# Kernel optimization log

Measured on AMD Instinct MI355X. Metric: run time of the kernel, lower is better.

Reference implementation:

```python
import jax, jax.numpy as jnp
import numpy as np

OBS_DIM, ACT_DIM, HID_DIM, FEAT = 256, 32, 1024, 512
T_STEPS, BATCH = 64, 512
LOG2PI = float(np.log(2.0 * np.pi))


def _mlp(h, w0, b0, w1, b1, w2, b2):
    # 2 hidden elu layers + linear head (MLPDecoder mean; fix_std Normal, std=1)
    x = jax.nn.elu(h @ w0.T + b0)
    x = jax.nn.elu(x @ w1.T + b1)
    return x @ w2.T + b2


def _gru(x, h, w_ih, w_hh, b_ih, b_hh):
    # torch.nn.GRUCell semantics
    gi = x @ w_ih.T + b_ih
    gh = h @ w_hh.T + b_hh
    i_r, i_z, i_n = jnp.split(gi, 3, axis=-1)
    h_r, h_z, h_n = jnp.split(gh, 3, axis=-1)
    r = jax.nn.sigmoid(i_r + h_r)
    z = jax.nn.sigmoid(i_z + h_z)
    n = jnp.tanh(i_n + r * h_n)
    return (1.0 - z) * n + z * h


def setup_inputs() -> dict:
    key = jax.random.key(0)
    ks = jax.random.split(key, 20)
    d = {}
    d['obs'] = jax.random.normal(ks[0], (T_STEPS, BATCH, OBS_DIM), jnp.float32)
    d['action'] = jax.random.normal(ks[1], (T_STEPS, BATCH, ACT_DIM), jnp.float32)
    d['reward'] = jax.random.normal(ks[2], (T_STEPS, BATCH, 1), jnp.float32)
    in_dim = OBS_DIM + ACT_DIM
    s = lambda fan_in: 1.0 / np.sqrt(fan_in)
    d['gru_w_ih'] = jax.random.normal(ks[3], (3 * HID_DIM, in_dim), jnp.float32) * s(in_dim)
    d['gru_w_hh'] = jax.random.normal(ks[4], (3 * HID_DIM, HID_DIM), jnp.float32) * s(HID_DIM)
    d['gru_b_ih'] = jnp.zeros((3 * HID_DIM,), jnp.float32)
    d['gru_b_hh'] = jnp.zeros((3 * HID_DIM,), jnp.float32)
    for name, out_dim, base in (('obs', OBS_DIM, 5), ('rew', 1, 11)):
        d[f'{name}_w0'] = jax.random.normal(ks[base], (FEAT, HID_DIM), jnp.float32) * s(HID_DIM)
        d[f'{name}_b0'] = jnp.zeros((FEAT,), jnp.float32)
        d[f'{name}_w1'] = jax.random.normal(ks[base + 1], (FEAT, FEAT), jnp.float32) * s(FEAT)
        d[f'{name}_b1'] = jnp.zeros((FEAT,), jnp.float32)
        d[f'{name}_w2'] = jax.random.normal(ks[base + 2], (out_dim, FEAT), jnp.float32) * s(FEAT)
        d[f'{name}_b2'] = jnp.zeros((out_dim,), jnp.float32)
    return d


def reference(obs, action, reward,
              gru_w_ih, gru_w_hh, gru_b_ih, gru_b_hh,
              obs_w0, obs_b0, obs_w1, obs_b1, obs_w2, obs_b2,
              rew_w0, rew_b0, rew_w1, rew_b1, rew_w2, rew_b2):
    T, B = obs.shape[0], obs.shape[1]

    def normal_logprob_sum(x, mean):
        # Normal(mean, std=1): -0.5*(x-mean)^2 - 0.5*log(2*pi), summed
        return -0.5 * jnp.sum((x - mean) ** 2 + LOG2PI)

    h0 = _gru(jnp.concatenate([obs[0], jnp.zeros_like(action[0])], axis=1),
              jnp.zeros((B, HID_DIM), obs.dtype),
              gru_w_ih, gru_w_hh, gru_b_ih, gru_b_hh)

    def step(h, xs):
        obs_t, act_t, rew_t = xs
        obs_mean = _mlp(h, obs_w0, obs_b0, obs_w1, obs_b1, obs_w2, obs_b2)
        lp_obs = normal_logprob_sum(obs_t, obs_mean)
        rew_mean = _mlp(h, rew_w0, rew_b0, rew_w1, rew_b1, rew_w2, rew_b2)
        lp_rew = normal_logprob_sum(rew_t, rew_mean)
        # feed predicted obs (mode) + ground-truth action back into the GRU
        x = jnp.concatenate([obs_mean, act_t], axis=1)
        h_next = _gru(x, h, gru_w_ih, gru_w_hh, gru_b_ih, gru_b_hh)
        return h_next, (obs_mean, rew_mean, lp_obs, lp_rew)

    _, (pre_obs, pre_reward, lp_obs, lp_rew) = jax.lax.scan(
        step, h0, (obs, action, reward))

    denom = jnp.asarray(T * B, obs.dtype)
    pre_obs_loss = -jnp.sum(lp_obs) / denom
    pre_reward_loss = -jnp.sum(lp_rew) / denom
    loss = pre_obs_loss + pre_reward_loss  # action_mimic=False -> action loss is 0
    return loss, pre_obs, pre_reward
```

## Files before the change

### kernel.cpp

```cpp
#include <hip/hip_runtime.h>
#include <stdint.h>

#define T_STEPS 64
#define BATCH   512
#define OBS_DIM 256
#define ACT_DIM 32
#define HID     1024
#define FEAT    512
#define GDIM    3072
#define KIH     288
#define NBLK    256
#define GMEMB   32
#define LOG2PI  1.8378770664093453f
#define HWREG_XCC_ID 14356

typedef __attribute__((ext_vector_type(8))) short  short8;
typedef __attribute__((ext_vector_type(4))) float  floatx4;
typedef __attribute__((ext_vector_type(4))) unsigned int uintx4;
typedef unsigned long long ull;

__device__ __forceinline__ float bf2f(unsigned int u) {
    return __uint_as_float(u << 16);
}
__device__ __forceinline__ unsigned int f2bf(float f) {
    unsigned int u = __float_as_uint(f);
    return (u + 0x7FFFu + ((u >> 16) & 1u)) >> 16;
}
__device__ __forceinline__ float elu1(float x)  { return x > 0.f ? x : expm1f(x); }
__device__ __forceinline__ float sigm(float x)  { return 1.f / (1.f + expf(-x)); }

__device__ __forceinline__ unsigned int dev_ld(const unsigned int* p) {
    return __hip_atomic_load(p, __ATOMIC_RELAXED, __HIP_MEMORY_SCOPE_AGENT);
}
__device__ __forceinline__ ull dev_ld64(const ull* p) {
    return __hip_atomic_load(p, __ATOMIC_RELAXED, __HIP_MEMORY_SCOPE_AGENT);
}
__device__ __forceinline__ void dev_st(unsigned int* p, unsigned int v) {
    __hip_atomic_store(p, v, __ATOMIC_RELAXED, __HIP_MEMORY_SCOPE_AGENT);
}
__device__ __forceinline__ float dev_ldf(const float* p) {
    return __uint_as_float(dev_ld((const unsigned int*)p));
}

template<bool COH>
__device__ __forceinline__ unsigned int a_ld(const unsigned int* p) {
    return COH ? dev_ld(p) : *p;
}
template<bool COH>
__device__ __forceinline__ ull a_ld64(const ull* p) {
    return COH ? dev_ld64(p) : *p;
}
template<bool COH>
__device__ __forceinline__ void a_st(unsigned int* p, unsigned int v) {
    if (COH) dev_st(p, v); else *p = v;
}

struct ParamsReal {
    const float* obs; const float* action; const float* reward;
    const float* b_ih; const float* b_hh;
    const float* b1o; const float* b1r; const float* b2o; const float* b2r;
    const unsigned short* Ws1; const unsigned short* Wih;
    const unsigned short* W1o; const unsigned short* W1r;
    const unsigned short* W2o; const unsigned short* w2r;
    const float* bias_s1;
    unsigned short* Z1[2]; unsigned short* Z2[2]; unsigned short* Xbuf[2];
    unsigned short* hbf[2]; unsigned short* GHb[2]; float* h[2];
    float* accum; float* out;
    int* bar;
};
#define P ParamsReal

__device__ __forceinline__ void bar_fast() {
    asm volatile("" ::: "memory");
    __builtin_amdgcn_s_barrier();
    asm volatile("" ::: "memory");
}
__device__ __forceinline__ void bar_lds() {
    asm volatile("s_waitcnt lgkmcnt(0)" ::: "memory");
    __builtin_amdgcn_s_barrier();
    asm volatile("" ::: "memory");
}

__device__ __forceinline__ void gbar(int* cnt, int* gen, int& epoch, int members) {
    __syncthreads();
    if (threadIdx.x == 0) {
        __builtin_amdgcn_fence(__ATOMIC_RELEASE, "workgroup");
        epoch++;
        int prev = __hip_atomic_fetch_add(cnt, 1, __ATOMIC_RELAXED,
                                          __HIP_MEMORY_SCOPE_AGENT);
        if (prev == members * epoch - 1) {
            __hip_atomic_store(gen, epoch, __ATOMIC_RELAXED,
                               __HIP_MEMORY_SCOPE_AGENT);
        } else {
            while (__hip_atomic_load(gen, __ATOMIC_RELAXED,
                                     __HIP_MEMORY_SCOPE_AGENT) < epoch)
                __builtin_amdgcn_s_sleep(2);
        }
        __builtin_amdgcn_fence(__ATOMIC_ACQUIRE, "workgroup");
    }
    __syncthreads();
}

template<bool COH>
__device__ __forceinline__ void s1_stage(const P& p, unsigned short* lds,
                                         int g, int m,
                                         const unsigned short* hbf_r,
                                         unsigned short* Z1_w,
                                         unsigned short* GHb_w) {
    const int tid = threadIdx.x, lane = tid & 63, wv = tid >> 6;
    const int wr = wv & 1, wc = wv >> 1, fr = lane & 15, fq = lane >> 4;
    const int rowg = g * 64, col0 = m * 128;
    unsigned short* ldsA = lds;
    unsigned short* ldsB = lds + 64 * 136;

    floatx4 acc[2][4];
    floatx4 z4 = {0.f, 0.f, 0.f, 0.f};
#pragma unroll
    for (int mi = 0; mi < 2; ++mi)
#pragma unroll
        for (int n = 0; n < 4; ++n) acc[mi][n] = z4;

    const ull* Aq = (const ull*)(hbf_r + (size_t)rowg * HID);
    const unsigned short* Bg = p.Ws1 + (size_t)col0 * HID;

    ull apf[8];
#pragma unroll
    for (int j = 0; j < 8; ++j) { int f = tid + 256 * j;
        apf[j] = a_ld64<COH>(Aq + (size_t)(f >> 5) * 256 + (f & 31)); }
    uintx4 rb0[4], rb1[4];
#pragma unroll
    for (int i = 0; i < 4; ++i) { int c = tid + 256 * i;
        const unsigned short* bp = Bg + (size_t)(c >> 3) * HID + ((c & 7) << 3);
        rb0[i] = __builtin_nontemporal_load((const uintx4*)bp);
        rb1[i] = __builtin_nontemporal_load((const uintx4*)(bp + 64)); }

#define S1_MFMA(ASUB)                                                          \
    {                                                                          \
        _Pragma("unroll")                                                      \
        for (int ks = 0; ks < 2; ++ks) {                                       \
            short8 af[2], bf8[4];                                              \
            _Pragma("unroll")                                                  \
            for (int mi = 0; mi < 2; ++mi)                                     \
                af[mi] = *(const short8*)(ldsA + (wr * 32 + mi * 16 + fr) * 136 + (ASUB) + ks * 32 + fq * 8); \
            _Pragma("unroll")                                                  \
            for (int n = 0; n < 4; ++n)                                        \
                bf8[n] = *(const short8*)(ldsB + (wc * 64 + n * 16 + fr) * 72 + ks * 32 + fq * 8); \
            _Pragma("unroll")                                                  \
            for (int mi = 0; mi < 2; ++mi)                                     \
                _Pragma("unroll")                                              \
                for (int n = 0; n < 4; ++n)                                    \
                    acc[mi][n] = __builtin_amdgcn_mfma_f32_16x16x32_bf16(      \
                        af[mi], bf8[n], acc[mi][n], 0, 0, 0);                  \
        }                                                                      \
    }

    for (int it2 = 0; it2 < 8; ++it2) {
        bar_fast();
#pragma unroll
        for (int j = 0; j < 8; ++j) { int f = tid + 256 * j;
            *(ull*)(ldsA + (size_t)(f >> 5) * 136 + ((f & 31) << 2)) = apf[j]; }
#pragma unroll
        for (int i = 0; i < 4; ++i) { int c = tid + 256 * i;
            *(uintx4*)(ldsB + (c >> 3) * 72 + ((c & 7) << 3)) = rb0[i]; }
        bar_lds();
        if (it2 < 7) {
            int c2 = it2 + 1;
#pragma unroll
            for (int j = 0; j < 8; ++j) { int f = tid + 256 * j;
                apf[j] = a_ld64<COH>(Aq + (size_t)(f >> 5) * 256 + c2 * 32 + (f & 31)); }
            int k0n = (2 * it2 + 2) * 64;
#pragma unroll
            for (int i = 0; i < 4; ++i) { int c = tid + 256 * i;
                rb0[i] = __builtin_nontemporal_load((const uintx4*)
                    (Bg + (size_t)(c >> 3) * HID + k0n + ((c & 7) << 3))); }
        }
        S1_MFMA(0);
        bar_fast();
#pragma unroll
        for (int i = 0; i < 4; ++i) { int c = tid + 256 * i;
            *(uintx4*)(ldsB + (c >> 3) * 72 + ((c & 7) << 3)) = rb1[i]; }
        bar_lds();
        if (it2 < 7) {
            int k0n = (2 * it2 + 3) * 64;
#pragma unroll
            for (int i = 0; i < 4; ++i) { int c = tid + 256 * i;
                rb1[i] = __builtin_nontemporal_load((const uintx4*)
                    (Bg + (size_t)(c >> 3) * HID + k0n + ((c & 7) << 3))); }
        }
        S1_MFMA(64);
    }
#undef S1_MFMA

    const bool isZ1 = (col0 < 1024);
#pragma unroll
    for (int mi = 0; mi < 2; ++mi)
#pragma unroll
        for (int n = 0; n < 4; ++n)
#pragma unroll
            for (int j = 0; j < 4; ++j) {
                int row = rowg + wr * 32 + mi * 16 + fq * 4 + j;
                int col = col0 + wc * 64 + n * 16 + fr;
                float v = acc[mi][n][j] + p.bias_s1[col];
                unsigned int ow = f2bf(isZ1 ? elu1(v) : v);
                unsigned int pr = __shfl_xor(ow, 1, 64);
                if (!(fr & 1)) {
                    unsigned int pk = ow | (pr << 16);
                    if (isZ1)
                        a_st<COH>((unsigned int*)(Z1_w + row * HID + col), pk);
                    else
                        a_st<COH>((unsigned int*)GHb_w + (size_t)row * 1536 + ((col - 1024) >> 1), pk);
                }
            }
}

template<bool COH>
__device__ __forceinline__ void s2_stage(const P& p, unsigned short* lds,
                                         int g, int m,
                                         const unsigned short* Z1_r,
                                         unsigned short* Z2_w) {
    const int tid = threadIdx.x, lane = tid & 63, wv = tid >> 6;
    const int wr = wv & 1, wc = wv >> 1, fr = lane & 15, fq = lane >> 4;
    const int rowg = g * 64;
    const int z = m >> 4, col0 = (m & 15) * 32;
    unsigned short* ldsA = lds;
    unsigned short* ldsB = lds + 64 * 136;

    floatx4 acc[2];
    floatx4 z4 = {0.f, 0.f, 0.f, 0.f};
    acc[0] = z4; acc[1] = z4;

    const ull* Aq = (const ull*)(Z1_r + (size_t)rowg * HID + z * FEAT);
    const unsigned short* Bg = (z ? p.W1r : p.W1o) + (size_t)col0 * FEAT;
    const float* bias = z ? p.b1r : p.b1o;

    ull apf[8];
#pragma unroll
    for (int j = 0; j < 8; ++j) { int f = tid + 256 * j;
        apf[j] = a_ld64<COH>(Aq + (size_t)(f >> 5) * 256 + (f & 31)); }
    const unsigned short* bp0 = Bg + (size_t)(tid >> 3) * FEAT + ((tid & 7) << 3);
    uintx4 rb0 = *(const uintx4*)(bp0);
    uintx4 rb1 = *(const uintx4*)(bp0 + 64);

#define S2_MFMA(ASUB)                                                          \
    {                                                                          \
        _Pragma("unroll")                                                      \
        for (int ks = 0; ks < 2; ++ks) {                                       \
            short8 bf8 = *(const short8*)(ldsB + (wc * 16 + fr) * 72 + ks * 32 + fq * 8); \
            _Pragma("unroll")                                                  \
            for (int mi = 0; mi < 2; ++mi) {                                   \
                short8 af = *(const short8*)(ldsA + (wr * 32 + mi * 16 + fr) * 136 + (ASUB) + ks * 32 + fq * 8); \
                acc[mi] = __builtin_amdgcn_mfma_f32_16x16x32_bf16(af, bf8, acc[mi], 0, 0, 0); \
            }                                                                  \
        }                                                                      \
    }

    for (int it2 = 0; it2 < 4; ++it2) {
        bar_fast();
#pragma unroll
        for (int j = 0; j < 8; ++j) { int f = tid + 256 * j;
            *(ull*)(ldsA + (size_t)(f >> 5) * 136 + ((f & 31) << 2)) = apf[j]; }
        *(uintx4*)(ldsB + (tid >> 3) * 72 + ((tid & 7) << 3)) = rb0;
        bar_lds();
        if (it2 < 3) {
            int c2 = it2 + 1;
#pragma unroll
            for (int j = 0; j < 8; ++j) { int f = tid + 256 * j;
                apf[j] = a_ld64<COH>(Aq + (size_t)(f >> 5) * 256 + c2 * 32 + (f & 31)); }
            rb0 = *(const uintx4*)(bp0 + (2 * it2 + 2) * 64);
        }
        S2_MFMA(0);
        bar_fast();
        *(uintx4*)(ldsB + (tid >> 3) * 72 + ((tid & 7) << 3)) = rb1;
        bar_lds();
        if (it2 < 3) rb1 = *(const uintx4*)(bp0 + (2 * it2 + 3) * 64);
        S2_MFMA(64);
    }
#undef S2_MFMA

#pragma unroll
    for (int mi = 0; mi < 2; ++mi)
#pragma unroll
        for (int j = 0; j < 4; ++j) {
            int row = rowg + wr * 32 + mi * 16 + fq * 4 + j;
            int col = col0 + wc * 16 + fr;
            float v = acc[mi][j] + bias[col];
            unsigned int ow = f2bf(elu1(v));
            unsigned int pr = __shfl_xor(ow, 1, 64);
            if (!(fr & 1))
                a_st<COH>((unsigned int*)(Z2_w + row * HID + z * FEAT + col), ow | (pr << 16));
        }
}

template<bool COH>
__device__ __forceinline__ void s3_stage(const P& p, unsigned short* lds,
                                         int g, int m, int t,
                                         const unsigned short* Z2_r,
                                         unsigned short* Xbuf_w) {
    const int tid = threadIdx.x, lane = tid & 63, wv = tid >> 6;
    const int wr = wv & 1, wc = wv >> 1, fr = lane & 15, fq = lane >> 4;
    const int rowg = g * 64;

    if (m < 8) {
        const int col0 = m * 32;
        unsigned short* ldsA = lds;
        unsigned short* ldsB = lds + 64 * 136;
        floatx4 acc[2];
        floatx4 z4 = {0.f, 0.f, 0.f, 0.f};
        acc[0] = z4; acc[1] = z4;

        const ull* Aq = (const ull*)(Z2_r + (size_t)rowg * HID);
        const unsigned short* Bg = p.W2o + (size_t)col0 * FEAT;

        ull apf[8];
#pragma unroll
        for (int j = 0; j < 8; ++j) { int f = tid + 256 * j;
            apf[j] = a_ld64<COH>(Aq + (size_t)(f >> 5) * 256 + (f & 31)); }
        const unsigned short* bp0 = Bg + (size_t)(tid >> 3) * FEAT + ((tid & 7) << 3);
        uintx4 rb0 = *(const uintx4*)(bp0);
        uintx4 rb1 = *(const uintx4*)(bp0 + 64);

#define S3_MFMA(ASUB)                                                          \
        {                                                                      \
            _Pragma("unroll")                                                  \
            for (int ks = 0; ks < 2; ++ks) {                                   \
                short8 bf8 = *(const short8*)(ldsB + (wc * 16 + fr) * 72 + ks * 32 + fq * 8); \
                _Pragma("unroll")                                              \
                for (int mi = 0; mi < 2; ++mi) {                               \
                    short8 af = *(const short8*)(ldsA + (wr * 32 + mi * 16 + fr) * 136 + (ASUB) + ks * 32 + fq * 8); \
                    acc[mi] = __builtin_amdgcn_mfma_f32_16x16x32_bf16(af, bf8, acc[mi], 0, 0, 0); \
                }                                                              \
            }                                                                  \
        }

        for (int it2 = 0; it2 < 4; ++it2) {
            bar_fast();
#pragma unroll
            for (int j = 0; j < 8; ++j) { int f = tid + 256 * j;
                *(ull*)(ldsA + (size_t)(f >> 5) * 136 + ((f & 31) << 2)) = apf[j]; }
            *(uintx4*)(ldsB + (tid >> 3) * 72 + ((tid & 7) << 3)) = rb0;
            bar_lds();
            if (it2 < 3) {
                int c2 = it2 + 1;
#pragma unroll
                for (int j = 0; j < 8; ++j) { int f = tid + 256 * j;
                    apf[j] = a_ld64<COH>(Aq + (size_t)(f >> 5) * 256 + c2 * 32 + (f & 31)); }
                rb0 = *(const uintx4*)(bp0 + (2 * it2 + 2) * 64);
            }
            S3_MFMA(0);
            bar_fast();
            *(uintx4*)(ldsB + (tid >> 3) * 72 + ((tid & 7) << 3)) = rb1;
            bar_lds();
            if (it2 < 3) rb1 = *(const uintx4*)(bp0 + (2 * it2 + 3) * 64);
            S3_MFMA(64);
        }
#undef S3_MFMA

        const int col = col0 + wc * 16 + fr;
        const float b2oc = p.b2o[col];
        float lsum = 0.f;
#pragma unroll
        for (int mi = 0; mi < 2; ++mi)
#pragma unroll
            for (int j = 0; j < 4; ++j) {
                int row = rowg + wr * 32 + mi * 16 + fq * 4 + j;
                float mval = acc[mi][j] + b2oc;
                size_t oidx = (size_t)t * BATCH * OBS_DIM + (size_t)row * OBS_DIM + col;
                __builtin_nontemporal_store(mval, p.out + 1 + oidx);
                unsigned int ow = f2bf(mval);
                unsigned int pr = __shfl_xor(ow, 1, 64);
                if (!(fr & 1))
                    a_st<COH>((unsigned int*)(Xbuf_w + row * KIH + col), ow | (pr << 16));
                float d = __builtin_nontemporal_load(p.obs + oidx) - mval;
                lsum += d * d;
            }
#pragma unroll
        for (int off = 32; off > 0; off >>= 1) lsum += __shfl_down(lsum, off, 64);
        if (lane == 0) atomicAdd(p.accum + 0, lsum);
    } else if (m == 8) {
        for (int e = tid; e < 64 * 16; e += 256) {
            int row = rowg + (e >> 4), cp = (e & 15) * 2;
            const float* ap = p.action + ((size_t)t * BATCH + row) * ACT_DIM + cp;
            unsigned int lo = f2bf(__builtin_nontemporal_load(ap));
            unsigned int hi = f2bf(__builtin_nontemporal_load(ap + 1));
            a_st<COH>((unsigned int*)(Xbuf_w + row * KIH + OBS_DIM + cp), lo | (hi << 16));
        }
    } else if (m >= 16) {
        const int row = rowg + (m - 16) * 4 + wv;
        const ull* zq = (const ull*)(Z2_r + (size_t)row * HID + FEAT) + lane * 2;
        ull z0 = a_ld64<COH>(zq);
        ull z1 = a_ld64<COH>(zq + 1);
        short8 w8 = *(const short8*)(p.w2r + lane * 8);
        float s = 0.f;
#pragma unroll
        for (int k = 0; k < 4; ++k) {
            unsigned int u = (unsigned int)(z0 >> (16 * k)) & 0xFFFFu;
            s += bf2f(u) * bf2f((unsigned int)(unsigned short)w8[k]);
        }
#pragma unroll
        for (int k = 0; k < 4; ++k) {
            unsigned int u = (unsigned int)(z1 >> (16 * k)) & 0xFFFFu;
            s += bf2f(u) * bf2f((unsigned int)(unsigned short)w8[4 + k]);
        }
#pragma unroll
        for (int off = 32; off > 0; off >>= 1) s += __shfl_down(s, off, 64);
        if (lane == 0) {
            float mm = s + p.b2r[0];
            __builtin_nontemporal_store(
                mm, p.out + 1 + (size_t)T_STEPS * BATCH * OBS_DIM + (size_t)t * BATCH + row);
            float d = __builtin_nontemporal_load(p.reward + (size_t)t * BATCH + row) - mm;
            atomicAdd(p.accum + 1, d * d);
        }
    }
}

template<bool COH>
__device__ __forceinline__ void s4_stage(const P& p, unsigned short* lds,
                                         int g, int m, int use_gh,
                                         const unsigned short* Xbuf_r,
                                         const unsigned short* GHb_r,
                                         const float* h_r,
                                         float* h_w, unsigned short* hbf_w) {
    const int tid = threadIdx.x, lane = tid & 63, wv = tid >> 6;
    const int wr = wv & 1, wc = wv >> 1, fr = lane & 15, fq = lane >> 4;
    const int rowg = g * 64;
    const int col0 = m * 32;
    unsigned short* ldsA = lds;
    unsigned short* ldsB = lds + 64 * 104;

    floatx4 acc[3][2];
    floatx4 z4 = {0.f, 0.f, 0.f, 0.f};
#pragma unroll
    for (int g3 = 0; g3 < 3; ++g3) { acc[g3][0] = z4; acc[g3][1] = z4; }

    const ull* Xq = (const ull*)(Xbuf_r + (size_t)rowg * KIH);
    ull apf[6];
#pragma unroll
    for (int j = 0; j < 6; ++j) { int f = tid + 256 * j;
        apf[j] = a_ld64<COH>(Xq + (size_t)(f / 24) * 72 + (f % 24)); }

    uintx4 wpfA[5], wpfB[5];
#pragma unroll
    for (int j = 0; j < 5; ++j) { int f = tid + 256 * j;
        if (f < 1152) { int r = f / 12, ko = (f - r * 12) * 8;
            const unsigned short* wp =
                p.Wih + (size_t)((r >> 5) * HID + col0 + (r & 31)) * KIH + ko;
            wpfA[j] = __builtin_nontemporal_load((const uintx4*)wp);
            wpfB[j] = __builtin_nontemporal_load((const uintx4*)(wp + 96)); } }

#pragma unroll
    for (int c = 0; c < 3; ++c) {
        bar_fast();
#pragma unroll
        for (int j = 0; j < 6; ++j) { int f = tid + 256 * j;
            *(ull*)(ldsA + (size_t)(f / 24) * 104 + ((f % 24) << 2)) = apf[j]; }
#pragma unroll
        for (int j = 0; j < 5; ++j) { int f = tid + 256 * j;
            if (f < 1152) { int r = f / 12, ko = (f - r * 12) * 8;
                *(uintx4*)(ldsB + r * 104 + ko) = (c & 1) ? wpfB[j] : wpfA[j]; } }
        bar_lds();
        if (c < 2) {
#pragma unroll
            for (int j = 0; j < 6; ++j) { int f = tid + 256 * j;
                apf[j] = a_ld64<COH>(Xq + (size_t)(f / 24) * 72 + (c + 1) * 24 + (f % 24)); }
        }
        if (c == 0) {
#pragma unroll
            for (int j = 0; j < 5; ++j) { int f = tid + 256 * j;
                if (f < 1152) { int r = f / 12, ko = (f - r * 12) * 8;
                    wpfA[j] = __builtin_nontemporal_load((const uintx4*)
                        (p.Wih + (size_t)((r >> 5) * HID + col0 + (r & 31)) * KIH + 192 + ko)); } }
        }
#pragma unroll
        for (int ks = 0; ks < 3; ++ks) {
            short8 af[2];
#pragma unroll
            for (int mi = 0; mi < 2; ++mi)
                af[mi] = *(const short8*)(ldsA + (wr * 32 + mi * 16 + fr) * 104 + ks * 32 + fq * 8);
#pragma unroll
            for (int g3 = 0; g3 < 3; ++g3) {
                short8 bf8 = *(const short8*)(ldsB + (g3 * 32 + wc * 16 + fr) * 104 + ks * 32 + fq * 8);
#pragma unroll
                for (int mi = 0; mi < 2; ++mi)
                    acc[g3][mi] = __builtin_amdgcn_mfma_f32_16x16x32_bf16(
                        af[mi], bf8, acc[g3][mi], 0, 0, 0);
            }
        }
    }

    const int col = col0 + wc * 16 + fr;
    const float bir = p.b_ih[col];
    const float biz = p.b_ih[HID + col];
    const float bin = p.b_ih[2 * HID + col];
    float hrv[2][4], hzv[2][4], hnv[2][4], hpv[2][4];
    if (use_gh) {
        const unsigned int* GW = (const unsigned int*)GHb_r;
        const int cw = col >> 1, hi = col & 1;
#pragma unroll
        for (int mi = 0; mi < 2; ++mi)
#pragma unroll
            for (int j = 0; j < 4; ++j) {
                int row = rowg + wr * 32 + mi * 16 + fq * 4 + j;
                unsigned int ur = a_ld<COH>(GW + (size_t)row * 1536 + cw);
                unsigned int uz = a_ld<COH>(GW + (size_t)row * 1536 + 512 + cw);
                unsigned int un = a_ld<COH>(GW + (size_t)row * 1536 + 1024 + cw);
                hrv[mi][j] = bf2f(hi ? (ur >> 16) : (ur & 0xFFFFu));
                hzv[mi][j] = bf2f(hi ? (uz >> 16) : (uz & 0xFFFFu));
                hnv[mi][j] = bf2f(hi ? (un >> 16) : (un & 0xFFFFu));
                hpv[mi][j] = __uint_as_float(a_ld<COH>((const unsigned int*)(h_r + (size_t)row * HID + col)));
            }
    } else {
        float br = p.b_hh[col], bz = p.b_hh[HID + col], bn = p.b_hh[2 * HID + col];
#pragma unroll
        for (int mi = 0; mi < 2; ++mi)
#pragma unroll
            for (int j = 0; j < 4; ++j) {
                hrv[mi][j] = br; hzv[mi][j] = bz; hnv[mi][j] = bn; hpv[mi][j] = 0.f;
            }
    }
#pragma unroll
    for (int mi = 0; mi < 2; ++mi)
#pragma unroll
        for (int j = 0; j < 4; ++j) {
            int row = rowg + wr * 32 + mi * 16 + fq * 4 + j;
            float r  = sigm(acc[0][mi][j] + bir + hrv[mi][j]);
            float z  = sigm(acc[1][mi][j] + biz + hzv[mi][j]);
            float nn = tanhf(acc[2][mi][j] + bin + r * hnv[mi][j]);
            float hv = (1.f - z) * nn + z * hpv[mi][j];
            a_st<COH>((unsigned int*)(h_w + (size_t)row * HID + col), __float_as_uint(hv));
            unsigned int ow = f2bf(hv);
            unsigned int pr = __shfl_xor(ow, 1, 64);
            if (!(fr & 1))
                a_st<COH>((unsigned int*)(hbf_w + row * HID + col), ow | (pr << 16));
        }
}

template<bool COH>
__device__ void rollout(const P& p, unsigned short* lds, int g, int m) {
    int* gcnt = p.bar + g * 128;
    int* ggen = p.bar + g * 128 + 64;
    int epoch = 0;

    s4_stage<COH>(p, lds, g, m, 0, p.Xbuf[1], p.GHb[0], p.h[0], p.h[0], p.hbf[0]);
    gbar(gcnt, ggen, epoch, GMEMB);

    for (int t = 0; t < T_STEPS; ++t) {
        const int pr = t & 1, nx = (t + 1) & 1;
        s1_stage<COH>(p, lds, g, m, p.hbf[pr], p.Z1[pr], p.GHb[pr]);
        gbar(gcnt, ggen, epoch, GMEMB);
        s2_stage<COH>(p, lds, g, m, p.Z1[pr], p.Z2[pr]);
        gbar(gcnt, ggen, epoch, GMEMB);
        s3_stage<COH>(p, lds, g, m, t, p.Z2[pr], p.Xbuf[pr]);
        gbar(gcnt, ggen, epoch, GMEMB);
        if (t < T_STEPS - 1) {
            s4_stage<COH>(p, lds, g, m, 1, p.Xbuf[pr], p.GHb[pr], p.h[pr],
                          p.h[nx], p.hbf[nx]);
            gbar(gcnt, ggen, epoch, GMEMB);
        }
    }
}

__global__ __launch_bounds__(256, 1) void k_persist(P p) {
    __shared__ unsigned short lds[17920];
    __shared__ int sh[3];

    const int bid = blockIdx.x;
    if (threadIdx.x == 0) {
        unsigned int xcd = __builtin_amdgcn_s_getreg(HWREG_XCC_ID) & 7u;
        int r = __hip_atomic_fetch_add(p.bar + 1024 + xcd, 1,
                                       __ATOMIC_RELAXED, __HIP_MEMORY_SCOPE_AGENT);
        sh[0] = (int)xcd; sh[1] = r;
    }
    int repoch = 0;
    gbar(p.bar + 1200, p.bar + 1264, repoch, NBLK);
    if (threadIdx.x == 0) {
        int ok = (sh[1] < 32);
        for (int i = 0; i < 8; ++i)
            ok &= (dev_ld((const unsigned int*)(p.bar + 1024 + i)) == 32u);
        sh[2] = ok;
    }
    __syncthreads();

    if (sh[2]) rollout<false>(p, lds, sh[0], sh[1]);
    else       rollout<true >(p, lds, bid & 7, bid >> 3);

    gbar(p.bar + 1200, p.bar + 1264, repoch, NBLK);
    if (bid == 0 && threadIdx.x == 0) {
        const float inv = 1.f / (float)(T_STEPS * BATCH);
        float a0 = dev_ldf(p.accum + 0);
        float a1 = dev_ldf(p.accum + 1);
        p.out[0] = 0.5f * a0 * inv + 128.f * LOG2PI
                 + 0.5f * a1 * inv + 0.5f * LOG2PI;
    }
}

__global__ void k_convert(
    const float* __restrict__ ow0, const float* __restrict__ rw0,
    const float* __restrict__ whh, const float* __restrict__ wih,
    const float* __restrict__ ow1, const float* __restrict__ rw1,
    const float* __restrict__ ow2, const float* __restrict__ rw2,
    const float* __restrict__ ob0, const float* __restrict__ rb0,
    const float* __restrict__ bhh,
    unsigned short* __restrict__ Ws1, unsigned short* __restrict__ Wih,
    unsigned short* __restrict__ W1o, unsigned short* __restrict__ W1r,
    unsigned short* __restrict__ W2o, unsigned short* __restrict__ w2r,
    float* __restrict__ bias_s1)
{
    const int i0 = blockIdx.x * 256 + threadIdx.x;
    const int stride = gridDim.x * 256;
    for (int i = i0; i < 4096 * 1024; i += stride) {
        int row = i >> 10;
        float v = (row < 512) ? ow0[i]
                : (row < 1024) ? rw0[i - 512 * 1024]
                               : whh[i - 1024 * 1024];
        Ws1[i] = (unsigned short)f2bf(v);
    }
    for (int i = i0; i < GDIM * KIH; i += stride) Wih[i] = (unsigned short)f2bf(wih[i]);
    for (int i = i0; i < FEAT * FEAT; i += stride) {
        W1o[i] = (unsigned short)f2bf(ow1[i]);
        W1r[i] = (unsigned short)f2bf(rw1[i]);
    }
    for (int i = i0; i < OBS_DIM * FEAT; i += stride) W2o[i] = (unsigned short)f2bf(ow2[i]);
    for (int i = i0; i < FEAT; i += stride) w2r[i] = (unsigned short)f2bf(rw2[i]);
    for (int i = i0; i < 4096; i += stride)
        bias_s1[i] = (i < 512) ? ob0[i] : (i < 1024) ? rb0[i - 512] : bhh[i - 1024];
}

__global__ void k_init(const float* __restrict__ obs,
                       unsigned short* __restrict__ Xbuf1,
                       float* __restrict__ accum,
                       int* __restrict__ bar)
{
    int i = blockIdx.x * 256 + threadIdx.x;
    if (i < BATCH * KIH) {
        int row = i / KIH, col = i - row * KIH;
        Xbuf1[i] = (col < OBS_DIM) ? (unsigned short)f2bf(obs[row * OBS_DIM + col])
                                   : (unsigned short)0;
    }
    if (i < 2)    accum[i] = 0.f;
    if (i < 1536) bar[i] = 0;
}

extern "C" void kernel_launch(void* const* d_in, const int* in_sizes, int n_in,
                              void* d_out, int out_size, void* d_ws, size_t ws_size,
                              hipStream_t stream)
{
    const float* obs      = (const float*)d_in[0];
    const float* action   = (const float*)d_in[1];
    const float* reward   = (const float*)d_in[2];
    const float* gru_w_ih = (const float*)d_in[3];
    const float* gru_w_hh = (const float*)d_in[4];
    const float* gru_b_ih = (const float*)d_in[5];
    const float* gru_b_hh = (const float*)d_in[6];
    const float* obs_w0   = (const float*)d_in[7];
    const float* obs_b0   = (const float*)d_in[8];
    const float* obs_w1   = (const float*)d_in[9];
    const float* obs_b1   = (const float*)d_in[10];
    const float* obs_w2   = (const float*)d_in[11];
    const float* obs_b2   = (const float*)d_in[12];
    const float* rew_w0   = (const float*)d_in[13];
    const float* rew_b0   = (const float*)d_in[14];
    const float* rew_w1   = (const float*)d_in[15];
    const float* rew_b1   = (const float*)d_in[16];
    const float* rew_w2   = (const float*)d_in[17];
    const float* rew_b2   = (const float*)d_in[18];

    char* ws = (char*)d_ws;
    auto alloc = [&](size_t bytes) -> char* {
        char* pr = ws;
        ws += (bytes + 255) & ~(size_t)255;
        return pr;
    };
    unsigned short* Ws1  = (unsigned short*)alloc((size_t)4096 * 1024 * 2);
    unsigned short* Wih  = (unsigned short*)alloc((size_t)GDIM * KIH * 2);
    unsigned short* W1o  = (unsigned short*)alloc((size_t)FEAT * FEAT * 2);
    unsigned short* W1r  = (unsigned short*)alloc((size_t)FEAT * FEAT * 2);
    unsigned short* W2o  = (unsigned short*)alloc((size_t)OBS_DIM * FEAT * 2);
    unsigned short* w2r  = (unsigned short*)alloc((size_t)FEAT * 2);
    float* bias_s1       = (float*)alloc((size_t)4096 * 4);
    unsigned short* Z1a  = (unsigned short*)alloc((size_t)BATCH * HID * 2);
    unsigned short* Z1b  = (unsigned short*)alloc((size_t)BATCH * HID * 2);
    unsigned short* Z2a  = (unsigned short*)alloc((size_t)BATCH * HID * 2);
    unsigned short* Z2b  = (unsigned short*)alloc((size_t)BATCH * HID * 2);
    unsigned short* GHa  = (unsigned short*)alloc((size_t)BATCH * GDIM * 2);
    unsigned short* GHbB = (unsigned short*)alloc((size_t)BATCH * GDIM * 2);
    unsigned short* Xba  = (unsigned short*)alloc((size_t)BATCH * KIH * 2);
    unsigned short* Xbb  = (unsigned short*)alloc((size_t)BATCH * KIH * 2);
    float* ha            = (float*)alloc((size_t)BATCH * HID * 4);
    float* hb            = (float*)alloc((size_t)BATCH * HID * 4);
    unsigned short* hfa  = (unsigned short*)alloc((size_t)BATCH * HID * 2);
    unsigned short* hfb  = (unsigned short*)alloc((size_t)BATCH * HID * 2);
    float* accum         = (float*)alloc(256);
    int*   bar           = (int*)alloc(8192);

    dim3 blk(256);

    k_convert<<<dim3(1024), blk, 0, stream>>>(
        obs_w0, rew_w0, gru_w_hh, gru_w_ih, obs_w1, rew_w1, obs_w2, rew_w2,
        obs_b0, rew_b0, gru_b_hh, Ws1, Wih, W1o, W1r, W2o, w2r, bias_s1);

    k_init<<<dim3((BATCH * KIH + 255) / 256), blk, 0, stream>>>(obs, Xbb, accum, bar);

    P hp;
    hp.obs = obs; hp.action = action; hp.reward = reward;
    hp.b_ih = gru_b_ih; hp.b_hh = gru_b_hh;
    hp.b1o = obs_b1; hp.b1r = rew_b1; hp.b2o = obs_b2; hp.b2r = rew_b2;
    hp.Ws1 = Ws1; hp.Wih = Wih; hp.W1o = W1o; hp.W1r = W1r;
    hp.W2o = W2o; hp.w2r = w2r; hp.bias_s1 = bias_s1;
    hp.Z1[0] = Z1a; hp.Z1[1] = Z1b;
    hp.Z2[0] = Z2a; hp.Z2[1] = Z2b;
    hp.Xbuf[0] = Xba; hp.Xbuf[1] = Xbb;
    hp.hbf[0] = hfa; hp.hbf[1] = hfb;
    hp.GHb[0] = GHa; hp.GHb[1] = GHbB;
    hp.h[0] = ha; hp.h[1] = hb;
    hp.accum = accum; hp.out = (float*)d_out;
    hp.bar = bar;

    k_persist<<<dim3(NBLK), blk, 0, stream>>>(hp);
}
```

Before: 2.542 ms.

## Double block threads, load B operands directly to registers, use flag-based group barrier

The persistent kernel now runs 512 threads per block instead of 256, so each wave owns a smaller MFMA tile. In the GEMM stages, weight fragments are loaded straight from global memory into registers in MFMA layout rather than staged through LDS. A-tiles are double-buffered in LDS, with fewer barriers per k-step and raised wave priority around the MFMA blocks. The atomic-counter group barrier is replaced by per-member epoch flags polled by one wave, removing contended atomics at the cost of more polling traffic and more register pressure per wave.

```diff
diff --git a/kernel.cpp b/kernel.cpp
--- a/kernel.cpp
+++ b/kernel.cpp
@@ -101,6 +101,22 @@
     __syncthreads();
 }
 
+__device__ __forceinline__ void gbar_flags(int* fbase, int m, int& epoch) {
+    __syncthreads();
+    epoch++;
+    if (threadIdx.x == 0) {
+        __builtin_amdgcn_fence(__ATOMIC_RELEASE, "workgroup");
+        dev_st((unsigned int*)(fbase + m * 16), (unsigned int)epoch);
+    }
+    if (threadIdx.x < 64) {
+        const unsigned int* fp =
+            (const unsigned int*)(fbase + (threadIdx.x & 31) * 16);
+        while ((int)dev_ld(fp) < epoch) __builtin_amdgcn_s_sleep(4);
+        __builtin_amdgcn_fence(__ATOMIC_ACQUIRE, "workgroup");
+    }
+    __syncthreads();
+}
+
 template<bool COH>
 __device__ __forceinline__ void s1_stage(const P& p, unsigned short* lds,
                                          int g, int m,
@@ -108,98 +124,105 @@
                                          unsigned short* Z1_w,
                                          unsigned short* GHb_w) {
     const int tid = threadIdx.x, lane = tid & 63, wv = tid >> 6;
-    const int wr = wv & 1, wc = wv >> 1, fr = lane & 15, fq = lane >> 4;
+    const int wr = wv & 1, wc = wv >> 1;
+    const int fr = lane & 15, fq = lane >> 4;
     const int rowg = g * 64, col0 = m * 128;
-    unsigned short* ldsA = lds;
-    unsigned short* ldsB = lds + 64 * 136;
-
-    floatx4 acc[2][4];
+    unsigned short* A0 = lds;
+    unsigned short* A1 = lds + 64 * 136;
+
+    floatx4 acc[2][2];
     floatx4 z4 = {0.f, 0.f, 0.f, 0.f};
+    acc[0][0] = z4; acc[0][1] = z4; acc[1][0] = z4; acc[1][1] = z4;
+
+    const ull* Aq = (const ull*)(hbf_r + (size_t)rowg * HID);
+    const unsigned short* Bb = p.Ws1 + (size_t)(col0 + wc * 32 + fr) * HID + fq * 8;
+
+    ull apf[4];
+#pragma unroll
+    for (int j = 0; j < 4; ++j) { int f = tid + 512 * j;
+        apf[j] = a_ld64<COH>(Aq + (size_t)(f >> 5) * 256 + (f & 31)); }
+
+    short8 b0[2][4], b1[2][4];
+#pragma unroll
+    for (int n = 0; n < 2; ++n)
+#pragma unroll
+        for (int ks = 0; ks < 4; ++ks) {
+            const unsigned short* bp = Bb + (size_t)n * 16 * HID + ks * 32;
+            b0[n][ks] = __builtin_nontemporal_load((const short8*)bp);
+            b1[n][ks] = __builtin_nontemporal_load((const short8*)(bp + 128));
+        }
+#pragma unroll
+    for (int j = 0; j < 4; ++j) { int f = tid + 512 * j;
+        *(ull*)(A0 + (size_t)(f >> 5) * 136 + ((f & 31) << 2)) = apf[j]; }
+#pragma unroll
+    for (int j = 0; j < 4; ++j) { int f = tid + 512 * j;
+        apf[j] = a_ld64<COH>(Aq + (size_t)(f >> 5) * 256 + 32 + (f & 31)); }
+    bar_lds();
+
+#define S1_MFMA(ABUF, BV)                                                      \
+    { __builtin_amdgcn_s_setprio(1);                                           \
+      _Pragma("unroll")                                                        \
+      for (int ks = 0; ks < 4; ++ks) {                                         \
+        short8 af0 = *(const short8*)((ABUF) + (wr * 32 + fr) * 136 + ks * 32 + fq * 8);      \
+        short8 af1 = *(const short8*)((ABUF) + (wr * 32 + 16 + fr) * 136 + ks * 32 + fq * 8); \
+        acc[0][0] = __builtin_amdgcn_mfma_f32_16x16x32_bf16(af0, BV[0][ks], acc[0][0], 0, 0, 0); \
+        acc[0][1] = __builtin_amdgcn_mfma_f32_16x16x32_bf16(af0, BV[1][ks], acc[0][1], 0, 0, 0); \
+        acc[1][0] = __builtin_amdgcn_mfma_f32_16x16x32_bf16(af1, BV[0][ks], acc[1][0], 0, 0, 0); \
+        acc[1][1] = __builtin_amdgcn_mfma_f32_16x16x32_bf16(af1, BV[1][ks], acc[1][1], 0, 0, 0); \
+      }                                                                        \
+      __builtin_amdgcn_s_setprio(0); }
+
+#pragma unroll 1
+    for (int it2 = 0; it2 < 4; ++it2) {
+        const int c = 2 * it2;
+#pragma unroll
+        for (int j = 0; j < 4; ++j) { int f = tid + 512 * j;
+            *(ull*)(A1 + (size_t)(f >> 5) * 136 + ((f & 31) << 2)) = apf[j]; }
+        if (it2 < 3) {
+#pragma unroll
+            for (int j = 0; j < 4; ++j) { int f = tid + 512 * j;
+                apf[j] = a_ld64<COH>(Aq + (size_t)(f >> 5) * 256 + (c + 2) * 32 + (f & 31)); }
+        }
+        S1_MFMA(A0, b0);
+        if (it2 < 3) {
+#pragma unroll
+            for (int n = 0; n < 2; ++n)
+#pragma unroll
+                for (int ks = 0; ks < 4; ++ks)
+                    b0[n][ks] = __builtin_nontemporal_load((const short8*)
+                        (Bb + (size_t)n * 16 * HID + (c + 2) * 128 + ks * 32));
+        }
+        bar_lds();
+        if (it2 < 3) {
+#pragma unroll
+            for (int j = 0; j < 4; ++j) { int f = tid + 512 * j;
+                *(ull*)(A0 + (size_t)(f >> 5) * 136 + ((f & 31) << 2)) = apf[j]; }
+#pragma unroll
+            for (int j = 0; j < 4; ++j) { int f = tid + 512 * j;
+                apf[j] = a_ld64<COH>(Aq + (size_t)(f >> 5) * 256 + (c + 3) * 32 + (f & 31)); }
+        }
+        S1_MFMA(A1, b1);
+        if (it2 < 3) {
+#pragma unroll
+            for (int n = 0; n < 2; ++n)
+#pragma unroll
+                for (int ks = 0; ks < 4; ++ks)
+                    b1[n][ks] = __builtin_nontemporal_load((const short8*)
+                        (Bb + (size_t)n * 16 * HID + (c + 3) * 128 + ks * 32));
+        }
+        bar_lds();
+    }
+#undef S1_MFMA
+
+    const bool isZ1 = (col0 < 1024);
 #pragma unroll
     for (int mi = 0; mi < 2; ++mi)
 #pragma unroll
-        for (int n = 0; n < 4; ++n) acc[mi][n] = z4;
-
-    const ull* Aq = (const ull*)(hbf_r + (size_t)rowg * HID);
-    const unsigned short* Bg = p.Ws1 + (size_t)col0 * HID;
-
-    ull apf[8];
-#pragma unroll
-    for (int j = 0; j < 8; ++j) { int f = tid + 256 * j;
-        apf[j] = a_ld64<COH>(Aq + (size_t)(f >> 5) * 256 + (f & 31)); }
-    uintx4 rb0[4], rb1[4];
-#pragma unroll
-    for (int i = 0; i < 4; ++i) { int c = tid + 256 * i;
-        const unsigned short* bp = Bg + (size_t)(c >> 3) * HID + ((c & 7) << 3);
-        rb0[i] = __builtin_nontemporal_load((const uintx4*)bp);
-        rb1[i] = __builtin_nontemporal_load((const uintx4*)(bp + 64)); }
-
-#define S1_MFMA(ASUB)                                                          \
-    {                                                                          \
-        _Pragma("unroll")                                                      \
-        for (int ks = 0; ks < 2; ++ks) {                                       \
-            short8 af[2], bf8[4];                                              \
-            _Pragma("unroll")                                                  \
-            for (int mi = 0; mi < 2; ++mi)                                     \
-                af[mi] = *(const short8*)(ldsA + (wr * 32 + mi * 16 + fr) * 136 + (ASUB) + ks * 32 + fq * 8); \
-            _Pragma("unroll")                                                  \
-            for (int n = 0; n < 4; ++n)                                        \
-                bf8[n] = *(const short8*)(ldsB + (wc * 64 + n * 16 + fr) * 72 + ks * 32 + fq * 8); \
-            _Pragma("unroll")                                                  \
-            for (int mi = 0; mi < 2; ++mi)                                     \
-                _Pragma("unroll")                                              \
-                for (int n = 0; n < 4; ++n)                                    \
-                    acc[mi][n] = __builtin_amdgcn_mfma_f32_16x16x32_bf16(      \
-                        af[mi], bf8[n], acc[mi][n], 0, 0, 0);                  \
-        }                                                                      \
-    }
-
-    for (int it2 = 0; it2 < 8; ++it2) {
-        bar_fast();
-#pragma unroll
-        for (int j = 0; j < 8; ++j) { int f = tid + 256 * j;
-            *(ull*)(ldsA + (size_t)(f >> 5) * 136 + ((f & 31) << 2)) = apf[j]; }
-#pragma unroll
-        for (int i = 0; i < 4; ++i) { int c = tid + 256 * i;
-            *(uintx4*)(ldsB + (c >> 3) * 72 + ((c & 7) << 3)) = rb0[i]; }
-        bar_lds();
-        if (it2 < 7) {
-            int c2 = it2 + 1;
-#pragma unroll
-            for (int j = 0; j < 8; ++j) { int f = tid + 256 * j;
-                apf[j] = a_ld64<COH>(Aq + (size_t)(f >> 5) * 256 + c2 * 32 + (f & 31)); }
-            int k0n = (2 * it2 + 2) * 64;
-#pragma unroll
-            for (int i = 0; i < 4; ++i) { int c = tid + 256 * i;
-                rb0[i] = __builtin_nontemporal_load((const uintx4*)
-                    (Bg + (size_t)(c >> 3) * HID + k0n + ((c & 7) << 3))); }
-        }
-        S1_MFMA(0);
-        bar_fast();
-#pragma unroll
-        for (int i = 0; i < 4; ++i) { int c = tid + 256 * i;
-            *(uintx4*)(ldsB + (c >> 3) * 72 + ((c & 7) << 3)) = rb1[i]; }
-        bar_lds();
-        if (it2 < 7) {
-            int k0n = (2 * it2 + 3) * 64;
-#pragma unroll
-            for (int i = 0; i < 4; ++i) { int c = tid + 256 * i;
-                rb1[i] = __builtin_nontemporal_load((const uintx4*)
-                    (Bg + (size_t)(c >> 3) * HID + k0n + ((c & 7) << 3))); }
-        }
-        S1_MFMA(64);
-    }
-#undef S1_MFMA
-
-    const bool isZ1 = (col0 < 1024);
-#pragma unroll
-    for (int mi = 0; mi < 2; ++mi)
-#pragma unroll
-        for (int n = 0; n < 4; ++n)
+        for (int n = 0; n < 2; ++n)
 #pragma unroll
             for (int j = 0; j < 4; ++j) {
                 int row = rowg + wr * 32 + mi * 16 + fq * 4 + j;
-                int col = col0 + wc * 64 + n * 16 + fr;
+                int col = col0 + wc * 32 + n * 16 + fr;
                 float v = acc[mi][n][j] + p.bias_s1[col];
                 unsigned int ow = f2bf(isZ1 ? elu1(v) : v);
                 unsigned int pr = __shfl_xor(ow, 1, 64);
@@ -219,76 +242,90 @@
                                          const unsigned short* Z1_r,
                                          unsigned short* Z2_w) {
     const int tid = threadIdx.x, lane = tid & 63, wv = tid >> 6;
-    const int wr = wv & 1, wc = wv >> 1, fr = lane & 15, fq = lane >> 4;
+    const int wr = wv & 3, wc = wv >> 2;
+    const int fr = lane & 15, fq = lane >> 4;
     const int rowg = g * 64;
     const int z = m >> 4, col0 = (m & 15) * 32;
-    unsigned short* ldsA = lds;
-    unsigned short* ldsB = lds + 64 * 136;
-
-    floatx4 acc[2];
-    floatx4 z4 = {0.f, 0.f, 0.f, 0.f};
-    acc[0] = z4; acc[1] = z4;
+    unsigned short* A0 = lds;
+    unsigned short* A1 = lds + 64 * 136;
+
+    floatx4 acc = {0.f, 0.f, 0.f, 0.f};
 
     const ull* Aq = (const ull*)(Z1_r + (size_t)rowg * HID + z * FEAT);
-    const unsigned short* Bg = (z ? p.W1r : p.W1o) + (size_t)col0 * FEAT;
+    const unsigned short* Bb = (z ? p.W1r : p.W1o) +
+                               (size_t)(col0 + wc * 16 + fr) * FEAT + fq * 8;
     const float* bias = z ? p.b1r : p.b1o;
 
-    ull apf[8];
-#pragma unroll
-    for (int j = 0; j < 8; ++j) { int f = tid + 256 * j;
+    ull apf[4];
+#pragma unroll
+    for (int j = 0; j < 4; ++j) { int f = tid + 512 * j;
         apf[j] = a_ld64<COH>(Aq + (size_t)(f >> 5) * 256 + (f & 31)); }
-    const unsigned short* bp0 = Bg + (size_t)(tid >> 3) * FEAT + ((tid & 7) << 3);
-    uintx4 rb0 = *(const uintx4*)(bp0);
-    uintx4 rb1 = *(const uintx4*)(bp0 + 64);
-
-#define S2_MFMA(ASUB)                                                          \
-    {                                                                          \
-        _Pragma("unroll")                                                      \
-        for (int ks = 0; ks < 2; ++ks) {                                       \
-            short8 bf8 = *(const short8*)(ldsB + (wc * 16 + fr) * 72 + ks * 32 + fq * 8); \
-            _Pragma("unroll")                                                  \
-            for (int mi = 0; mi < 2; ++mi) {                                   \
-                short8 af = *(const short8*)(ldsA + (wr * 32 + mi * 16 + fr) * 136 + (ASUB) + ks * 32 + fq * 8); \
-                acc[mi] = __builtin_amdgcn_mfma_f32_16x16x32_bf16(af, bf8, acc[mi], 0, 0, 0); \
-            }                                                                  \
-        }                                                                      \
-    }
-
-    for (int it2 = 0; it2 < 4; ++it2) {
-        bar_fast();
-#pragma unroll
-        for (int j = 0; j < 8; ++j) { int f = tid + 256 * j;
-            *(ull*)(ldsA + (size_t)(f >> 5) * 136 + ((f & 31) << 2)) = apf[j]; }
-        *(uintx4*)(ldsB + (tid >> 3) * 72 + ((tid & 7) << 3)) = rb0;
+    short8 b0[4], b1[4];
+#pragma unroll
+    for (int ks = 0; ks < 4; ++ks) {
+        b0[ks] = *(const short8*)(Bb + ks * 32);
+        b1[ks] = *(const short8*)(Bb + 128 + ks * 32);
+    }
+#pragma unroll
+    for (int j = 0; j < 4; ++j) { int f = tid + 512 * j;
+        *(ull*)(A0 + (size_t)(f >> 5) * 136 + ((f & 31) << 2)) = apf[j]; }
+#pragma unroll
+    for (int j = 0; j < 4; ++j) { int f = tid + 512 * j;
+        apf[j] = a_ld64<COH>(Aq + (size_t)(f >> 5) * 256 + 32 + (f & 31)); }
+    bar_lds();
+
+#define S23_MFMA(ABUF, BV)                                                     \
+    { _Pragma("unroll")                                                        \
+      for (int ks = 0; ks < 4; ++ks) {                                         \
+        short8 af = *(const short8*)((ABUF) + (wr * 16 + fr) * 136 + ks * 32 + fq * 8); \
+        acc = __builtin_amdgcn_mfma_f32_16x16x32_bf16(af, BV[ks], acc, 0, 0, 0); \
+      } }
+
+#pragma unroll 1
+    for (int it2 = 0; it2 < 2; ++it2) {
+        const int c = 2 * it2;
+#pragma unroll
+        for (int j = 0; j < 4; ++j) { int f = tid + 512 * j;
+            *(ull*)(A1 + (size_t)(f >> 5) * 136 + ((f & 31) << 2)) = apf[j]; }
+        if (it2 < 1) {
+#pragma unroll
+            for (int j = 0; j < 4; ++j) { int f = tid + 512 * j;
+                apf[j] = a_ld64<COH>(Aq + (size_t)(f >> 5) * 256 + (c + 2) * 32 + (f & 31)); }
+        }
+        S23_MFMA(A0, b0);
+        if (it2 < 1) {
+#pragma unroll
+            for (int ks = 0; ks < 4; ++ks)
+                b0[ks] = *(const short8*)(Bb + (c + 2) * 128 + ks * 32);
+        }
         bar_lds();
-        if (it2 < 3) {
-            int c2 = it2 + 1;
-#pragma unroll
-            for (int j = 0; j < 8; ++j) { int f = tid + 256 * j;
-                apf[j] = a_ld64<COH>(Aq + (size_t)(f >> 5) * 256 + c2 * 32 + (f & 31)); }
-            rb0 = *(const uintx4*)(bp0 + (2 * it2 + 2) * 64);
-        }
-        S2_MFMA(0);
-        bar_fast();
-        *(uintx4*)(ldsB + (tid >> 3) * 72 + ((tid & 7) << 3)) = rb1;
+        if (it2 < 1) {
+#pragma unroll
+            for (int j = 0; j < 4; ++j) { int f = tid + 512 * j;
+                *(ull*)(A0 + (size_t)(f >> 5) * 136 + ((f & 31) << 2)) = apf[j]; }
+#pragma unroll
+            for (int j = 0; j < 4; ++j) { int f = tid + 512 * j;
+                apf[j] = a_ld64<COH>(Aq + (size_t)(f >> 5) * 256 + (c + 3) * 32 + (f & 31)); }
+        }
+        S23_MFMA(A1, b1);
+        if (it2 < 1) {
+#pragma unroll
+            for (int ks = 0; ks < 4; ++ks)
+                b1[ks] = *(const short8*)(Bb + (c + 3) * 128 + ks * 32);
+        }
         bar_lds();
-        if (it2 < 3) rb1 = *(const uintx4*)(bp0 + (2 * it2 + 3) * 64);
-        S2_MFMA(64);
-    }
-#undef S2_MFMA
-
-#pragma unroll
-    for (int mi = 0; mi < 2; ++mi)
-#pragma unroll
-        for (int j = 0; j < 4; ++j) {
-            int row = rowg + wr * 32 + mi * 16 + fq * 4 + j;
-            int col = col0 + wc * 16 + fr;
-            float v = acc[mi][j] + bias[col];
-            unsigned int ow = f2bf(elu1(v));
-            unsigned int pr = __shfl_xor(ow, 1, 64);
-            if (!(fr & 1))
-                a_st<COH>((unsigned int*)(Z2_w + row * HID + z * FEAT + col), ow | (pr << 16));
-        }
+    }
+
+#pragma unroll
+    for (int j = 0; j < 4; ++j) {
+        int row = rowg + wr * 16 + fq * 4 + j;
+        int col = col0 + wc * 16 + fr;
+        float v = acc[j] + bias[col];
+        unsigned int ow = f2bf(elu1(v));
+        unsigned int pr = __shfl_xor(ow, 1, 64);
+        if (!(fr & 1))
+            a_st<COH>((unsigned int*)(Z2_w + row * HID + z * FEAT + col), ow | (pr << 16));
+    }
 }
 
 template<bool COH>
@@ -297,95 +334,101 @@
                                          const unsigned short* Z2_r,
                                          unsigned short* Xbuf_w) {
     const int tid = threadIdx.x, lane = tid & 63, wv = tid >> 6;
-    const int wr = wv & 1, wc = wv >> 1, fr = lane & 15, fq = lane >> 4;
+    const int wr = wv & 3, wc = wv >> 2;
+    const int fr = lane & 15, fq = lane >> 4;
     const int rowg = g * 64;
 
     if (m < 8) {
         const int col0 = m * 32;
-        unsigned short* ldsA = lds;
-        unsigned short* ldsB = lds + 64 * 136;
-        floatx4 acc[2];
-        floatx4 z4 = {0.f, 0.f, 0.f, 0.f};
-        acc[0] = z4; acc[1] = z4;
+        unsigned short* A0 = lds;
+        unsigned short* A1 = lds + 64 * 136;
+        floatx4 acc = {0.f, 0.f, 0.f, 0.f};
 
         const ull* Aq = (const ull*)(Z2_r + (size_t)rowg * HID);
-        const unsigned short* Bg = p.W2o + (size_t)col0 * FEAT;
-
-        ull apf[8];
-#pragma unroll
-        for (int j = 0; j < 8; ++j) { int f = tid + 256 * j;
+        const unsigned short* Bb = p.W2o + (size_t)(col0 + wc * 16 + fr) * FEAT + fq * 8;
+
+        ull apf[4];
+#pragma unroll
+        for (int j = 0; j < 4; ++j) { int f = tid + 512 * j;
             apf[j] = a_ld64<COH>(Aq + (size_t)(f >> 5) * 256 + (f & 31)); }
-        const unsigned short* bp0 = Bg + (size_t)(tid >> 3) * FEAT + ((tid & 7) << 3);
-        uintx4 rb0 = *(const uintx4*)(bp0);
-        uintx4 rb1 = *(const uintx4*)(bp0 + 64);
-
-#define S3_MFMA(ASUB)                                                          \
-        {                                                                      \
-            _Pragma("unroll")                                                  \
-            for (int ks = 0; ks < 2; ++ks) {                                   \
-                short8 bf8 = *(const short8*)(ldsB + (wc * 16 + fr) * 72 + ks * 32 + fq * 8); \
-                _Pragma("unroll")                                              \
-                for (int mi = 0; mi < 2; ++mi) {                               \
-                    short8 af = *(const short8*)(ldsA + (wr * 32 + mi * 16 + fr) * 136 + (ASUB) + ks * 32 + fq * 8); \
-                    acc[mi] = __builtin_amdgcn_mfma_f32_16x16x32_bf16(af, bf8, acc[mi], 0, 0, 0); \
-                }                                                              \
-            }                                                                  \
-        }
-
-        for (int it2 = 0; it2 < 4; ++it2) {
-            bar_fast();
-#pragma unroll
-            for (int j = 0; j < 8; ++j) { int f = tid + 256 * j;
-                *(ull*)(ldsA + (size_t)(f >> 5) * 136 + ((f & 31) << 2)) = apf[j]; }
-            *(uintx4*)(ldsB + (tid >> 3) * 72 + ((tid & 7) << 3)) = rb0;
+        short8 b0[4], b1[4];
+#pragma unroll
+        for (int ks = 0; ks < 4; ++ks) {
+            b0[ks] = *(const short8*)(Bb + ks * 32);
+            b1[ks] = *(const short8*)(Bb + 128 + ks * 32);
+        }
+#pragma unroll
+        for (int j = 0; j < 4; ++j) { int f = tid + 512 * j;
+            *(ull*)(A0 + (size_t)(f >> 5) * 136 + ((f & 31) << 2)) = apf[j]; }
+#pragma unroll
+        for (int j = 0; j < 4; ++j) { int f = tid + 512 * j;
+            apf[j] = a_ld64<COH>(Aq + (size_t)(f >> 5) * 256 + 32 + (f & 31)); }
+        bar_lds();
+
+#pragma unroll 1
+        for (int it2 = 0; it2 < 2; ++it2) {
+            const int c = 2 * it2;
+#pragma unroll
+            for (int j = 0; j < 4; ++j) { int f = tid + 512 * j;
+                *(ull*)(A1 + (size_t)(f >> 5) * 136 + ((f & 31) << 2)) = apf[j]; }
+            if (it2 < 1) {
+#pragma unroll
+                for (int j = 0; j < 4; ++j) { int f = tid + 512 * j;
+                    apf[j] = a_ld64<COH>(Aq + (size_t)(f >> 5) * 256 + (c + 2) * 32 + (f & 31)); }
+            }
+            S23_MFMA(A0, b0);
+            if (it2 < 1) {
+#pragma unroll
+                for (int ks = 0; ks < 4; ++ks)
+                    b0[ks] = *(const short8*)(Bb + (c + 2) * 128 + ks * 32);
+            }
             bar_lds();
-            if (it2 < 3) {
-                int c2 = it2 + 1;
-#pragma unroll
-                for (int j = 0; j < 8; ++j) { int f = tid + 256 * j;
-                    apf[j] = a_ld64<COH>(Aq + (size_t)(f >> 5) * 256 + c2 * 32 + (f & 31)); }
-                rb0 = *(const uintx4*)(bp0 + (2 * it2 + 2) * 64);
+            if (it2 < 1) {
+#pragma unroll
+                for (int j = 0; j < 4; ++j) { int f = tid + 512 * j;
+                    *(ull*)(A0 + (size_t)(f >> 5) * 136 + ((f & 31) << 2)) = apf[j]; }
+#pragma unroll
+                for (int j = 0; j < 4; ++j) { int f = tid + 512 * j;
+                    apf[j] = a_ld64<COH>(Aq + (size_t)(f >> 5) * 256 + (c + 3) * 32 + (f & 31)); }
             }
-            S3_MFMA(0);
-            bar_fast();
-            *(uintx4*)(ldsB + (tid >> 3) * 72 + ((tid & 7) << 3)) = rb1;
+            S23_MFMA(A1, b1);
+            if (it2 < 1) {
+#pragma unroll
+                for (int ks = 0; ks < 4; ++ks)
+                    b1[ks] = *(const short8*)(Bb + (c + 3) * 128 + ks * 32);
+            }
             bar_lds();
-            if (it2 < 3) rb1 = *(const uintx4*)(bp0 + (2 * it2 + 3) * 64);
-            S3_MFMA(64);
-        }
-#undef S3_MFMA
+        }
 
         const int col = col0 + wc * 16 + fr;
         const float b2oc = p.b2o[col];
         float lsum = 0.f;
 #pragma unroll
-        for (int mi = 0; mi < 2; ++mi)
-#pragma unroll
-            for (int j = 0; j < 4; ++j) {
-                int row = rowg + wr * 32 + mi * 16 + fq * 4 + j;
-                float mval = acc[mi][j] + b2oc;
-                size_t oidx = (size_t)t * BATCH * OBS_DIM + (size_t)row * OBS_DIM + col;
-                __builtin_nontemporal_store(mval, p.out + 1 + oidx);
-                unsigned int ow = f2bf(mval);
-                unsigned int pr = __shfl_xor(ow, 1, 64);
-                if (!(fr & 1))
-                    a_st<COH>((unsigned int*)(Xbuf_w + row * KIH + col), ow | (pr << 16));
-                float d = __builtin_nontemporal_load(p.obs + oidx) - mval;
-                lsum += d * d;
-            }
+        for (int j = 0; j < 4; ++j) {
+            int row = rowg + wr * 16 + fq * 4 + j;
+            float mval = acc[j] + b2oc;
+            size_t oidx = (size_t)t * BATCH * OBS_DIM + (size_t)row * OBS_DIM + col;
+            __builtin_nontemporal_store(mval, p.out + 1 + oidx);
+            unsigned int ow = f2bf(mval);
+            unsigned int pr = __shfl_xor(ow, 1, 64);
+            if (!(fr & 1))
+                a_st<COH>((unsigned int*)(Xbuf_w + row * KIH + col), ow | (pr << 16));
+            float d = __builtin_nontemporal_load(p.obs + oidx) - mval;
+            lsum += d * d;
+        }
 #pragma unroll
         for (int off = 32; off > 0; off >>= 1) lsum += __shfl_down(lsum, off, 64);
         if (lane == 0) atomicAdd(p.accum + 0, lsum);
     } else if (m == 8) {
-        for (int e = tid; e < 64 * 16; e += 256) {
+        for (int e = tid; e < 64 * 16; e += 512) {
             int row = rowg + (e >> 4), cp = (e & 15) * 2;
             const float* ap = p.action + ((size_t)t * BATCH + row) * ACT_DIM + cp;
             unsigned int lo = f2bf(__builtin_nontemporal_load(ap));
             unsigned int hi = f2bf(__builtin_nontemporal_load(ap + 1));
             a_st<COH>((unsigned int*)(Xbuf_w + row * KIH + OBS_DIM + cp), lo | (hi << 16));
         }
-    } else if (m >= 16) {
-        const int row = rowg + (m - 16) * 4 + wv;
+    } else if (m >= 16 && m < 24) {
+        const int row = rowg + (m - 16) * 8 + wv;
         const ull* zq = (const ull*)(Z2_r + (size_t)row * HID + FEAT) + lane * 2;
         ull z0 = a_ld64<COH>(zq);
         ull z1 = a_ld64<COH>(zq + 1);
@@ -421,26 +464,26 @@
                                          const float* h_r,
                                          float* h_w, unsigned short* hbf_w) {
     const int tid = threadIdx.x, lane = tid & 63, wv = tid >> 6;
-    const int wr = wv & 1, wc = wv >> 1, fr = lane & 15, fq = lane >> 4;
+    const int wr = wv & 3, wc = wv >> 2;
+    const int fr = lane & 15, fq = lane >> 4;
     const int rowg = g * 64;
     const int col0 = m * 32;
     unsigned short* ldsA = lds;
     unsigned short* ldsB = lds + 64 * 104;
 
-    floatx4 acc[3][2];
+    floatx4 acc[3];
     floatx4 z4 = {0.f, 0.f, 0.f, 0.f};
-#pragma unroll
-    for (int g3 = 0; g3 < 3; ++g3) { acc[g3][0] = z4; acc[g3][1] = z4; }
+    acc[0] = z4; acc[1] = z4; acc[2] = z4;
 
     const ull* Xq = (const ull*)(Xbuf_r + (size_t)rowg * KIH);
-    ull apf[6];
-#pragma unroll
-    for (int j = 0; j < 6; ++j) { int f = tid + 256 * j;
+    ull apf[3];
+#pragma unroll
+    for (int j = 0; j < 3; ++j) { int f = tid + 512 * j;
         apf[j] = a_ld64<COH>(Xq + (size_t)(f / 24) * 72 + (f % 24)); }
 
-    uintx4 wpfA[5], wpfB[5];
-#pragma unroll
-    for (int j = 0; j < 5; ++j) { int f = tid + 256 * j;
+    uintx4 wpfA[3], wpfB[3];
+#pragma unroll
+    for (int j = 0; j < 3; ++j) { int f = tid + 512 * j;
         if (f < 1152) { int r = f / 12, ko = (f - r * 12) * 8;
             const unsigned short* wp =
                 p.Wih + (size_t)((r >> 5) * HID + col0 + (r & 31)) * KIH + ko;
@@ -451,38 +494,32 @@
     for (int c = 0; c < 3; ++c) {
         bar_fast();
 #pragma unroll
-        for (int j = 0; j < 6; ++j) { int f = tid + 256 * j;
+        for (int j = 0; j < 3; ++j) { int f = tid + 512 * j;
             *(ull*)(ldsA + (size_t)(f / 24) * 104 + ((f % 24) << 2)) = apf[j]; }
 #pragma unroll
-        for (int j = 0; j < 5; ++j) { int f = tid + 256 * j;
+        for (int j = 0; j < 3; ++j) { int f = tid + 512 * j;
             if (f < 1152) { int r = f / 12, ko = (f - r * 12) * 8;
                 *(uintx4*)(ldsB + r * 104 + ko) = (c & 1) ? wpfB[j] : wpfA[j]; } }
         bar_lds();
         if (c < 2) {
 #pragma unroll
-            for (int j = 0; j < 6; ++j) { int f = tid + 256 * j;
+            for (int j = 0; j < 3; ++j) { int f = tid + 512 * j;
                 apf[j] = a_ld64<COH>(Xq + (size_t)(f / 24) * 72 + (c + 1) * 24 + (f % 24)); }
         }
         if (c == 0) {
 #pragma unroll
-            for (int j = 0; j < 5; ++j) { int f = tid + 256 * j;
+            for (int j = 0; j < 3; ++j) { int f = tid + 512 * j;
                 if (f < 1152) { int r = f / 12, ko = (f - r * 12) * 8;
                     wpfA[j] = __builtin_nontemporal_load((const uintx4*)
                         (p.Wih + (size_t)((r >> 5) * HID + col0 + (r & 31)) * KIH + 192 + ko)); } }
         }
 #pragma unroll
         for (int ks = 0; ks < 3; ++ks) {
-            short8 af[2];
-#pragma unroll
-            for (int mi = 0; mi < 2; ++mi)
-                af[mi] = *(const short8*)(ldsA + (wr * 32 + mi * 16 + fr) * 104 + ks * 32 + fq * 8);
+            short8 af = *(const short8*)(ldsA + (wr * 16 + fr) * 104 + ks * 32 + fq * 8);
 #pragma unroll
             for (int g3 = 0; g3 < 3; ++g3) {
                 short8 bf8 = *(const short8*)(ldsB + (g3 * 32 + wc * 16 + fr) * 104 + ks * 32 + fq * 8);
-#pragma unroll
-                for (int mi = 0; mi < 2; ++mi)
-                    acc[g3][mi] = __builtin_amdgcn_mfma_f32_16x16x32_bf16(
-                        af[mi], bf8, acc[g3][mi], 0, 0, 0);
+                acc[g3] = __builtin_amdgcn_mfma_f32_16x16x32_bf16(af, bf8, acc[g3], 0, 0, 0);
             }
         }
     }
@@ -491,76 +528,69 @@
     const float bir = p.b_ih[col];
     const float biz = p.b_ih[HID + col];
     const float bin = p.b_ih[2 * HID + col];
-    float hrv[2][4], hzv[2][4], hnv[2][4], hpv[2][4];
+    float hrv[4], hzv[4], hnv[4], hpv[4];
     if (use_gh) {
         const unsigned int* GW = (const unsigned int*)GHb_r;
         const int cw = col >> 1, hi = col & 1;
 #pragma unroll
-        for (int mi = 0; mi < 2; ++mi)
-#pragma unroll
-            for (int j = 0; j < 4; ++j) {
-                int row = rowg + wr * 32 + mi * 16 + fq * 4 + j;
-                unsigned int ur = a_ld<COH>(GW + (size_t)row * 1536 + cw);
-                unsigned int uz = a_ld<COH>(GW + (size_t)row * 1536 + 512 + cw);
-                unsigned int un = a_ld<COH>(GW + (size_t)row * 1536 + 1024 + cw);
-                hrv[mi][j] = bf2f(hi ? (ur >> 16) : (ur & 0xFFFFu));
-                hzv[mi][j] = bf2f(hi ? (uz >> 16) : (uz & 0xFFFFu));
-                hnv[mi][j] = bf2f(hi ? (un >> 16) : (un & 0xFFFFu));
-                hpv[mi][j] = __uint_as_float(a_ld<COH>((const unsigned int*)(h_r + (size_t)row * HID + col)));
-            }
+        for (int j = 0; j < 4; ++j) {
+            int row = rowg + wr * 16 + fq * 4 + j;
+            unsigned int ur = a_ld<COH>(GW + (size_t)row * 1536 + cw);
+            unsigned int uz = a_ld<COH>(GW + (size_t)row * 1536 + 512 + cw);
+            unsigned int un = a_ld<COH>(GW + (size_t)row * 1536 + 1024 + cw);
+            hrv[j] = bf2f(hi ? (ur >> 16) : (ur & 0xFFFFu));
+            hzv[j] = bf2f(hi ? (uz >> 16) : (uz & 0xFFFFu));
+            hnv[j] = bf2f(hi ? (un >> 16) : (un & 0xFFFFu));
+            hpv[j] = __uint_as_float(a_ld<COH>((const unsigned int*)(h_r + (size_t)row * HID + col)));
+        }
     } else {
         float br = p.b_hh[col], bz = p.b_hh[HID + col], bn = p.b_hh[2 * HID + col];
 #pragma unroll
-        for (int mi = 0; mi < 2; ++mi)
-#pragma unroll
-            for (int j = 0; j < 4; ++j) {
-                hrv[mi][j] = br; hzv[mi][j] = bz; hnv[mi][j] = bn; hpv[mi][j] = 0.f;
-            }
-    }
-#pragma unroll
-    for (int mi = 0; mi < 2; ++mi)
-#pragma unroll
         for (int j = 0; j < 4; ++j) {
-            int row = rowg + wr * 32 + mi * 16 + fq * 4 + j;
-            float r  = sigm(acc[0][mi][j] + bir + hrv[mi][j]);
-            float z  = sigm(acc[1][mi][j] + biz + hzv[mi][j]);
-            float nn = tanhf(acc[2][mi][j] + bin + r * hnv[mi][j]);
-            float hv = (1.f - z) * nn + z * hpv[mi][j];
-            a_st<COH>((unsigned int*)(h_w + (size_t)row * HID + col), __float_as_uint(hv));
-            unsigned int ow = f2bf(hv);
-            unsigned int pr = __shfl_xor(ow, 1, 64);
-            if (!(fr & 1))
-                a_st<COH>((unsigned int*)(hbf_w + row * HID + col), ow | (pr << 16));
-        }
+            hrv[j] = br; hzv[j] = bz; hnv[j] = bn; hpv[j] = 0.f;
+        }
+    }
+#pragma unroll
+    for (int j = 0; j < 4; ++j) {
+        int row = rowg + wr * 16 + fq * 4 + j;
+        float r  = sigm(acc[0][j] + bir + hrv[j]);
+        float z  = sigm(acc[1][j] + biz + hzv[j]);
+        float nn = tanhf(acc[2][j] + bin + r * hnv[j]);
+        float hv = (1.f - z) * nn + z * hpv[j];
+        a_st<COH>((unsigned int*)(h_w + (size_t)row * HID + col), __float_as_uint(hv));
+        unsigned int ow = f2bf(hv);
+        unsigned int pr = __shfl_xor(ow, 1, 64);
+        if (!(fr & 1))
+            a_st<COH>((unsigned int*)(hbf_w + row * HID + col), ow | (pr << 16));
+    }
 }
 
 template<bool COH>
 __device__ void rollout(const P& p, unsigned short* lds, int g, int m) {
-    int* gcnt = p.bar + g * 128;
-    int* ggen = p.bar + g * 128 + 64;
-    int epoch = 0;
+    int* fbase = p.bar + 2048 + g * 512;
+    int fep = 0;
 
     s4_stage<COH>(p, lds, g, m, 0, p.Xbuf[1], p.GHb[0], p.h[0], p.h[0], p.hbf[0]);
-    gbar(gcnt, ggen, epoch, GMEMB);
+    gbar_flags(fbase, m, fep);
 
     for (int t = 0; t < T_STEPS; ++t) {
         const int pr = t & 1, nx = (t + 1) & 1;
         s1_stage<COH>(p, lds, g, m, p.hbf[pr], p.Z1[pr], p.GHb[pr]);
-        gbar(gcnt, ggen, epoch, GMEMB);
+        gbar_flags(fbase, m, fep);
         s2_stage<COH>(p, lds, g, m, p.Z1[pr], p.Z2[pr]);
-        gbar(gcnt, ggen, epoch, GMEMB);
+        gbar_flags(fbase, m, fep);
         s3_stage<COH>(p, lds, g, m, t, p.Z2[pr], p.Xbuf[pr]);
-        gbar(gcnt, ggen, epoch, GMEMB);
+        gbar_flags(fbase, m, fep);
         if (t < T_STEPS - 1) {
             s4_stage<COH>(p, lds, g, m, 1, p.Xbuf[pr], p.GHb[pr], p.h[pr],
                           p.h[nx], p.hbf[nx]);
-            gbar(gcnt, ggen, epoch, GMEMB);
-        }
-    }
-}
-
-__global__ __launch_bounds__(256, 1) void k_persist(P p) {
-    __shared__ unsigned short lds[17920];
+            gbar_flags(fbase, m, fep);
+        }
+    }
+}
+
+__global__ __launch_bounds__(512, 1) void k_persist(P p) {
+    __shared__ unsigned short lds[17408];
     __shared__ int sh[3];
 
     const int bid = blockIdx.x;
@@ -637,7 +667,7 @@
                                    : (unsigned short)0;
     }
     if (i < 2)    accum[i] = 0.f;
-    if (i < 1536) bar[i] = 0;
+    if (i < 8192) bar[i] = 0;
 }
 
 extern "C" void kernel_launch(void* const* d_in, const int* in_sizes, int n_in,
@@ -690,15 +720,13 @@
     unsigned short* hfa  = (unsigned short*)alloc((size_t)BATCH * HID * 2);
     unsigned short* hfb  = (unsigned short*)alloc((size_t)BATCH * HID * 2);
     float* accum         = (float*)alloc(256);
-    int*   bar           = (int*)alloc(8192);
-
-    dim3 blk(256);
-
-    k_convert<<<dim3(1024), blk, 0, stream>>>(
+    int*   bar           = (int*)alloc(32768);
+
+    k_convert<<<dim3(1024), dim3(256), 0, stream>>>(
         obs_w0, rew_w0, gru_w_hh, gru_w_ih, obs_w1, rew_w1, obs_w2, rew_w2,
         obs_b0, rew_b0, gru_b_hh, Ws1, Wih, W1o, W1r, W2o, w2r, bias_s1);
 
-    k_init<<<dim3((BATCH * KIH + 255) / 256), blk, 0, stream>>>(obs, Xbb, accum, bar);
+    k_init<<<dim3((BATCH * KIH + 255) / 256), dim3(256), 0, stream>>>(obs, Xbb, accum, bar);
 
     P hp;
     hp.obs = obs; hp.action = action; hp.reward = reward;
@@ -715,5 +743,5 @@
     hp.accum = accum; hp.out = (float*)d_out;
     hp.bar = bar;
 
-    k_persist<<<dim3(NBLK), blk, 0, stream>>>(hp);
-}
+    k_persist<<<dim3(NBLK), dim3(512), 0, stream>>>(hp);
+}
```

After: 3.508 ms. +38.0%, slower.
